# Kernel tuning notes

Measured on AMD Instinct MI355X. Metric: run time of the kernel, lower is better.

## Reference

```python
import jax, jax.numpy as jnp
import numpy as np

EPS = 1e-6
NUM_HEADS = 16


def _layer_norm(x, alpha, beta):
    # Custom LN: unbiased std, divides by (std + eps) -- matches source exactly.
    mean = jnp.mean(x, axis=-1, keepdims=True)
    std = jnp.std(x, axis=-1, keepdims=True, ddof=1)
    return alpha * (x - mean) / (std + EPS) + beta


def _mha(x, wq, bq, wk, bk, wv, bv, wo, bo):
    B, S, D = x.shape
    H = NUM_HEADS
    Dh = D // H
    q = (x @ wq.T + bq).reshape(B, S, H, Dh)
    k = (x @ wk.T + bk).reshape(B, S, H, Dh)
    v = (x @ wv.T + bv).reshape(B, S, H, Dh)
    scores = jnp.einsum('bqhd,bkhd->bhqk', q, k) / jnp.sqrt(jnp.float32(Dh)).astype(x.dtype)
    p = jax.nn.softmax(scores, axis=-1)
    out = jnp.einsum('bhqk,bkhd->bqhd', p, v).reshape(B, S, D)
    return out @ wo.T + bo


def _ffn(x, w1, b1, w2, b2):
    return jax.nn.relu(x @ w1.T + b1) @ w2.T + b2


def setup_inputs() -> dict:
    key = jax.random.key(0)
    ks = jax.random.split(key, 8)
    B, S, D, Hf = 8, 1024, 1024, 4096
    s = lambda d: 1.0 / np.sqrt(d)
    return {
        'x': jax.random.normal(ks[0], (B, S, D), jnp.float32),
        'src_mask': jnp.ones((B, 1, 1, S), jnp.int32),
        'wq': jax.random.normal(ks[1], (D, D), jnp.float32) * s(D),
        'bq': jnp.zeros((D,), jnp.float32),
        'wk': jax.random.normal(ks[2], (D, D), jnp.float32) * s(D),
        'bk': jnp.zeros((D,), jnp.float32),
        'wv': jax.random.normal(ks[3], (D, D), jnp.float32) * s(D),
        'bv': jnp.zeros((D,), jnp.float32),
        'wo': jax.random.normal(ks[4], (D, D), jnp.float32) * s(D),
        'bo': jnp.zeros((D,), jnp.float32),
        'w1': jax.random.normal(ks[5], (Hf, D), jnp.float32) * s(D),
        'b1': jnp.zeros((Hf,), jnp.float32),
        'w2': jax.random.normal(ks[6], (D, Hf), jnp.float32) * s(Hf),
        'b2': jnp.zeros((D,), jnp.float32),
        'alpha': jnp.ones((D,), jnp.float32),
        'beta': jnp.zeros((D,), jnp.float32),
    }


def reference(x, src_mask, wq, bq, wk, bk, wv, bv, wo, bo, w1, b1, w2, b2, alpha, beta):
    # src_mask is unused in the source's attention implementation (faithful).
    # Pre-LN residual block 1: attention (shared LN params alpha/beta).
    x = x + _mha(_layer_norm(x, alpha, beta), wq, bq, wk, bk, wv, bv, wo, bo)
    # Pre-LN residual block 2: feed-forward (same shared LN instance).
    x = x + _ffn(_layer_norm(x, alpha, beta), w1, b1, w2, b2)
    return x
```

## Files before the change

### kernel.cpp

```cpp
#include <hip/hip_runtime.h>
#include <hip/hip_bf16.h>
#include <stdint.h>

typedef __bf16 bf16;
typedef __attribute__((ext_vector_type(8))) __bf16 bf16x8;
typedef __attribute__((ext_vector_type(4))) __bf16 bf16x4;
typedef __attribute__((ext_vector_type(4))) float floatx4;

typedef __attribute__((address_space(3))) uint32_t* lds_u32p;
typedef const __attribute__((address_space(1))) uint32_t* glb_u32p;

__device__ __forceinline__ void gload16(void* lds, const void* g) {
  __builtin_amdgcn_global_load_lds((glb_u32p)(uintptr_t)g,
                                   (lds_u32p)(uintptr_t)lds, 16, 0, 0);
}

__global__ __launch_bounds__(256) void detect_kernel(
    const unsigned short* __restrict__ xr, int* __restrict__ flag) {
  __shared__ int cnt;
  if (threadIdx.x == 0) cnt = 0;
  __syncthreads();
  int c = 0;
  for (int i = threadIdx.x; i < 8192; i += 256) {
    unsigned short e = (xr[i] >> 7) & 0xFF;
    if (e >= 0x90) ++c;
  }
  atomicAdd(&cnt, c);
  __syncthreads();
  if (threadIdx.x == 0) *flag = (cnt > 64) ? 1 : 0;
}

#define NCONV 14
struct ConvArgs {
  const void* src[NCONV];
  bf16* dst[NCONV];
  int nelem[NCONV];
  int bstart[NCONV + 1];
};

__global__ __launch_bounds__(256) void convert_kernel(ConvArgs a, const int* __restrict__ flag) {
  const int isf = *flag;
  const int bx = blockIdx.x;
  int t = 0;
  #pragma unroll
  for (int i = 1; i < NCONV; ++i)
    if (bx >= a.bstart[i]) t = i;
  const int base = (bx - a.bstart[t]) * 2048 + threadIdx.x * 8;
  if (base >= a.nelem[t]) return;
  if (isf) {
    const float* s = (const float*)a.src[t] + base;
    const float4 x0 = *reinterpret_cast<const float4*>(s);
    const float4 x1 = *reinterpret_cast<const float4*>(s + 4);
    bf16x8 o;
    o[0] = (bf16)x0.x; o[1] = (bf16)x0.y; o[2] = (bf16)x0.z; o[3] = (bf16)x0.w;
    o[4] = (bf16)x1.x; o[5] = (bf16)x1.y; o[6] = (bf16)x1.z; o[7] = (bf16)x1.w;
    *reinterpret_cast<bf16x8*>(a.dst[t] + base) = o;
  } else {
    *reinterpret_cast<bf16x8*>(a.dst[t] + base) =
        *reinterpret_cast<const bf16x8*>((const bf16*)a.src[t] + base);
  }
}

__global__ __launch_bounds__(256) void ln_kernel(
    const void* __restrict__ x, const bf16* __restrict__ alpha,
    const bf16* __restrict__ beta, bf16* __restrict__ y,
    const int* __restrict__ flag, int x_ext) {
  const int isf = *flag;
  const int row = blockIdx.x;
  const int tid = threadIdx.x;

  float v0, v1, v2, v3;
  if (x_ext && isf) {
    const float4 xv = *reinterpret_cast<const float4*>(
        (const float*)x + (size_t)row * 1024 + tid * 4);
    v0 = xv.x; v1 = xv.y; v2 = xv.z; v3 = xv.w;
  } else {
    const bf16x4 xv = *reinterpret_cast<const bf16x4*>(
        (const bf16*)x + (size_t)row * 1024 + tid * 4);
    v0 = (float)xv[0]; v1 = (float)xv[1]; v2 = (float)xv[2]; v3 = (float)xv[3];
  }
  float s = v0 + v1 + v2 + v3;
  float ss = v0 * v0 + v1 * v1 + v2 * v2 + v3 * v3;
  #pragma unroll
  for (int off = 32; off > 0; off >>= 1) {
    s += __shfl_down(s, off);
    ss += __shfl_down(ss, off);
  }
  __shared__ float red[8];
  __shared__ float s_mean, s_inv;
  const int w = tid >> 6, lane = tid & 63;
  if (lane == 0) { red[w] = s; red[4 + w] = ss; }
  __syncthreads();
  if (tid == 0) {
    float S = red[0] + red[1] + red[2] + red[3];
    float SS = red[4] + red[5] + red[6] + red[7];
    float mean = S * (1.0f / 1024.0f);
    float var = (SS - 1024.0f * mean * mean) * (1.0f / 1023.0f);
    var = fmaxf(var, 0.0f);
    s_mean = mean;
    s_inv = 1.0f / (sqrtf(var) + 1e-6f);
  }
  __syncthreads();
  const float mean = s_mean, inv = s_inv;
  const bf16x4 av = *reinterpret_cast<const bf16x4*>(alpha + tid * 4);
  const bf16x4 bv = *reinterpret_cast<const bf16x4*>(beta + tid * 4);
  bf16x4 out;
  out[0] = (bf16)((float)av[0] * (v0 - mean) * inv + (float)bv[0]);
  out[1] = (bf16)((float)av[1] * (v1 - mean) * inv + (float)bv[1]);
  out[2] = (bf16)((float)av[2] * (v2 - mean) * inv + (float)bv[2]);
  out[3] = (bf16)((float)av[3] * (v3 - mean) * inv + (float)bv[3]);
  *reinterpret_cast<bf16x4*>(y + (size_t)row * 1024 + tid * 4) = out;
}

template <bool RELU, bool RES>
__global__ __launch_bounds__(256) void gemm_bt(
    const bf16* __restrict__ A, const bf16* __restrict__ W,
    const bf16* __restrict__ bias, const void* __restrict__ res,
    void* __restrict__ C, int M, int N, int K,
    const int* __restrict__ flag, int res_ext, int out_ext, int row0) {
  __shared__ bf16 As[128 * 64];
  __shared__ bf16 Bs[128 * 64];
  const int isf = *flag;
  const int tid = threadIdx.x;
  const int m0 = blockIdx.x * 128, n0 = blockIdx.y * 128;
  const int wave = tid >> 6, lane = tid & 63;
  const int wm = (wave >> 1) * 64, wn = (wave & 1) * 64;
  const int lrow = lane & 15, quad = lane >> 4;

  const int srow = lane >> 3;
  const int gchunk = (lane & 7) ^ srow;
  const bf16* Ab = A + (size_t)m0 * K;
  const bf16* Wb = W + (size_t)n0 * K;

  floatx4 acc[4][4] = {};

  for (int k0 = 0; k0 < K; k0 += 64) {
    __syncthreads();
    #pragma unroll
    for (int t = 0; t < 4; ++t) {
      const int r = t * 32 + wave * 8;
      gload16(&As[r * 64], Ab + (size_t)(r + srow) * K + k0 + gchunk * 8);
      gload16(&Bs[r * 64], Wb + (size_t)(r + srow) * K + k0 + gchunk * 8);
    }
    __syncthreads();

    #pragma unroll
    for (int ks = 0; ks < 2; ++ks) {
      const int cswz = ((ks * 4 + quad) ^ (lrow & 7)) * 8;
      bf16x8 af[4], bw[4];
      #pragma unroll
      for (int i = 0; i < 4; ++i) {
        af[i] = *reinterpret_cast<const bf16x8*>(&As[(wm + i * 16 + lrow) * 64 + cswz]);
        bw[i] = *reinterpret_cast<const bf16x8*>(&Bs[(wn + i * 16 + lrow) * 64 + cswz]);
      }
      #pragma unroll
      for (int i = 0; i < 4; ++i)
        #pragma unroll
        for (int j = 0; j < 4; ++j)
          acc[i][j] = __builtin_amdgcn_mfma_f32_16x16x32_bf16(af[i], bw[j], acc[i][j], 0, 0, 0);
    }
  }

  #pragma unroll
  for (int j = 0; j < 4; ++j) {
    const int col = n0 + wn + j * 16 + lrow;
    const float bv = (float)bias[col];
    #pragma unroll
    for (int i = 0; i < 4; ++i) {
      #pragma unroll
      for (int r = 0; r < 4; ++r) {
        const int row = m0 + wm + i * 16 + quad * 4 + r;
        float v = acc[i][j][r] + bv;
        if (RELU) v = fmaxf(v, 0.0f);
        if (RES) {
          const size_t ridx = (size_t)row * N + col;
          v += (res_ext && isf) ? ((const float*)res)[ridx]
                                : (float)((const bf16*)res)[ridx];
        }
        const size_t oidx = (size_t)(row0 + row) * N + col;
        if (out_ext && isf) ((float*)C)[oidx] = v;
        else ((bf16*)C)[oidx] = (bf16)v;
      }
    }
  }
}

template <bool RELU, bool RES>
__global__ __launch_bounds__(256) void gemm_n64(
    const bf16* __restrict__ A, const bf16* __restrict__ W,
    const bf16* __restrict__ bias, const void* __restrict__ res,
    void* __restrict__ C, int M, int N, int K,
    const int* __restrict__ flag, int res_ext, int out_ext, int row0) {
  __shared__ bf16 As[128 * 64];
  __shared__ bf16 Bs[64 * 64];
  const int isf = *flag;
  const int tid = threadIdx.x;
  const int m0 = blockIdx.x * 128, n0 = blockIdx.y * 64;
  const int wave = tid >> 6, lane = tid & 63;
  const int wm = (wave >> 1) * 64, wn = (wave & 1) * 32;
  const int lrow = lane & 15, quad = lane >> 4;

  const int srow = lane >> 3;
  const int gchunk = (lane & 7) ^ srow;
  const bf16* Ab = A + (size_t)m0 * K;
  const bf16* Wb = W + (size_t)n0 * K;

  floatx4 acc[4][2] = {};

  for (int k0 = 0; k0 < K; k0 += 64) {
    __syncthreads();
    #pragma unroll
    for (int t = 0; t < 4; ++t) {
      const int r = t * 32 + wave * 8;
      gload16(&As[r * 64], Ab + (size_t)(r + srow) * K + k0 + gchunk * 8);
    }
    #pragma unroll
    for (int t = 0; t < 2; ++t) {
      const int r = t * 32 + wave * 8;
      gload16(&Bs[r * 64], Wb + (size_t)(r + srow) * K + k0 + gchunk * 8);
    }
    __syncthreads();

    #pragma unroll
    for (int ks = 0; ks < 2; ++ks) {
      const int cswz = ((ks * 4 + quad) ^ (lrow & 7)) * 8;
      bf16x8 af[4], bw[2];
      #pragma unroll
      for (int i = 0; i < 4; ++i)
        af[i] = *reinterpret_cast<const bf16x8*>(&As[(wm + i * 16 + lrow) * 64 + cswz]);
      #pragma unroll
      for (int j = 0; j < 2; ++j)
        bw[j] = *reinterpret_cast<const bf16x8*>(&Bs[(wn + j * 16 + lrow) * 64 + cswz]);
      #pragma unroll
      for (int i = 0; i < 4; ++i)
        #pragma unroll
        for (int j = 0; j < 2; ++j)
          acc[i][j] = __builtin_amdgcn_mfma_f32_16x16x32_bf16(af[i], bw[j], acc[i][j], 0, 0, 0);
    }
  }

  #pragma unroll
  for (int j = 0; j < 2; ++j) {
    const int col = n0 + wn + j * 16 + lrow;
    const float bv = (float)bias[col];
    #pragma unroll
    for (int i = 0; i < 4; ++i) {
      #pragma unroll
      for (int r = 0; r < 4; ++r) {
        const int row = m0 + wm + i * 16 + quad * 4 + r;
        float v = acc[i][j][r] + bv;
        if (RELU) v = fmaxf(v, 0.0f);
        if (RES) {
          const size_t ridx = (size_t)row * N + col;
          v += (res_ext && isf) ? ((const float*)res)[ridx]
                                : (float)((const bf16*)res)[ridx];
        }
        const size_t oidx = (size_t)(row0 + row) * N + col;
        if (out_ext && isf) ((float*)C)[oidx] = v;
        else ((bf16*)C)[oidx] = (bf16)v;
      }
    }
  }
}

__global__ __launch_bounds__(512, 2) void gemm_ffn1_256(
    const bf16* __restrict__ A, const bf16* __restrict__ W,
    const bf16* __restrict__ bias, bf16* __restrict__ C) {
  constexpr int K = 1024, N = 4096, NK = K / 64;
  __shared__ bf16 As[2][256 * 64];
  __shared__ bf16 Bs[2][256 * 64];
  const int tid = threadIdx.x;
  const int wave = tid >> 6, lane = tid & 63;
  const int m0 = blockIdx.x * 256, n0 = blockIdx.y * 256;
  const int wm = (wave >> 2) * 128;
  const int wn = (wave & 3) * 64;
  const int lrow = lane & 15, quad = lane >> 4;
  const int srow = lane >> 3;
  const int gchunk = (lane & 7) ^ srow;
  const bf16* Ab = A + (size_t)m0 * K;
  const bf16* Wb = W + (size_t)n0 * K;
  const int awr = wave * 32;

  floatx4 acc[8][4] = {};

  auto piece = [&](int kt, int nb, int p) {
    const bf16* G = (p < 2) ? Ab : Wb;
    bf16* L = (p < 2) ? &As[nb][0] : &Bs[nb][0];
    #pragma unroll
    for (int t = (p & 1) * 2; t < (p & 1) * 2 + 2; ++t) {
      const int r = awr + t * 8;
      gload16(L + r * 64, G + (size_t)(r + srow) * K + kt * 64 + gchunk * 8);
    }
  };

  piece(0, 0, 0); piece(0, 0, 1); piece(0, 0, 2); piece(0, 0, 3);

  for (int kt = 0; kt < NK; ++kt) {
    const int cur = kt & 1, nb = cur ^ 1;
    const bool pre = (kt + 1 < NK);

    __builtin_amdgcn_sched_barrier(0);
    __builtin_amdgcn_s_barrier();
    __builtin_amdgcn_sched_barrier(0);
    if (pre) {
      piece(kt + 1, nb, 0);
      asm volatile("s_waitcnt vmcnt(2)" ::: "memory");
    } else {
      asm volatile("s_waitcnt vmcnt(0)" ::: "memory");
    }
    __builtin_amdgcn_sched_barrier(0);
    __builtin_amdgcn_s_barrier();
    __builtin_amdgcn_sched_barrier(0);

    bf16x8 bw[4][2];
    #pragma unroll
    for (int j = 0; j < 4; ++j) {
      const int row = wn + j * 16 + lrow;
      #pragma unroll
      for (int ks = 0; ks < 2; ++ks) {
        const int c = (ks * 4 + quad) ^ (lrow & 7);
        bw[j][ks] = *reinterpret_cast<const bf16x8*>(&Bs[cur][row * 64 + c * 8]);
      }
    }
    #pragma unroll
    for (int p = 0; p < 4; ++p) {
      bf16x8 af[2][2];
      #pragma unroll
      for (int il = 0; il < 2; ++il) {
        const int row = wm + (p * 2 + il) * 16 + lrow;
        #pragma unroll
        for (int ks = 0; ks < 2; ++ks) {
          const int c = (ks * 4 + quad) ^ (lrow & 7);
          af[il][ks] = *reinterpret_cast<const bf16x8*>(&As[cur][row * 64 + c * 8]);
        }
      }
      if (pre && p < 3) piece(kt + 1, nb, p + 1);
      __builtin_amdgcn_s_setprio(1);
      #pragma unroll
      for (int il = 0; il < 2; ++il)
        #pragma unroll
        for (int j = 0; j < 4; ++j)
          #pragma unroll
          for (int ks = 0; ks < 2; ++ks)
            acc[p * 2 + il][j] = __builtin_amdgcn_mfma_f32_16x16x32_bf16(
                af[il][ks], bw[j][ks], acc[p * 2 + il][j], 0, 0, 0);
      __builtin_amdgcn_s_setprio(0);
    }
  }

  #pragma unroll
  for (int j = 0; j < 4; ++j) {
    const int col = n0 + wn + j * 16 + lrow;
    const float bv = (float)bias[col];
    #pragma unroll
    for (int i = 0; i < 8; ++i) {
      #pragma unroll
      for (int r = 0; r < 4; ++r) {
        const int row = m0 + wm + i * 16 + quad * 4 + r;
        C[(size_t)row * N + col] = (bf16)fmaxf(acc[i][j][r] + bv, 0.0f);
      }
    }
  }
}

__global__ __launch_bounds__(512, 2) void gemm_qkv256(
    const bf16* __restrict__ A, const bf16* __restrict__ W,
    const bf16* __restrict__ bias,
    bf16* __restrict__ Oq, bf16* __restrict__ Ok, bf16* __restrict__ Ov) {
  constexpr int K = 1024, NK = K / 64;
  __shared__ bf16 As[2][256 * 64];
  __shared__ bf16 Bs[2][256 * 64];
  const int tid = threadIdx.x;
  const int wave = tid >> 6, lane = tid & 63;
  const int m0 = blockIdx.x * 256, n0 = blockIdx.y * 256;
  const int wm = (wave >> 2) * 128;
  const int wn = (wave & 3) * 64;
  const int lrow = lane & 15, quad = lane >> 4;
  const int srow = lane >> 3;
  const int gchunk = (lane & 7) ^ srow;
  const bf16* Ab = A + (size_t)m0 * K;
  const bf16* Wb = W + (size_t)n0 * K;
  const int awr = wave * 32;

  floatx4 acc[8][4] = {};

  auto piece = [&](int kt, int nb, int p) {
    const bf16* G = (p < 2) ? Ab : Wb;
    bf16* L = (p < 2) ? &As[nb][0] : &Bs[nb][0];
    #pragma unroll
    for (int t = (p & 1) * 2; t < (p & 1) * 2 + 2; ++t) {
      const int r = awr + t * 8;
      gload16(L + r * 64, G + (size_t)(r + srow) * K + kt * 64 + gchunk * 8);
    }
  };

  piece(0, 0, 0); piece(0, 0, 1); piece(0, 0, 2); piece(0, 0, 3);

  for (int kt = 0; kt < NK; ++kt) {
    const int cur = kt & 1, nb = cur ^ 1;
    const bool pre = (kt + 1 < NK);

    __builtin_amdgcn_sched_barrier(0);
    __builtin_amdgcn_s_barrier();
    __builtin_amdgcn_sched_barrier(0);
    if (pre) {
      piece(kt + 1, nb, 0);
      asm volatile("s_waitcnt vmcnt(2)" ::: "memory");
    } else {
      asm volatile("s_waitcnt vmcnt(0)" ::: "memory");
    }
    __builtin_amdgcn_sched_barrier(0);
    __builtin_amdgcn_s_barrier();
    __builtin_amdgcn_sched_barrier(0);

    bf16x8 bw[4][2];
    #pragma unroll
    for (int j = 0; j < 4; ++j) {
      const int row = wn + j * 16 + lrow;
      #pragma unroll
      for (int ks = 0; ks < 2; ++ks) {
        const int c = (ks * 4 + quad) ^ (lrow & 7);
        bw[j][ks] = *reinterpret_cast<const bf16x8*>(&Bs[cur][row * 64 + c * 8]);
      }
    }
    #pragma unroll
    for (int p = 0; p < 4; ++p) {
      bf16x8 af[2][2];
      #pragma unroll
      for (int il = 0; il < 2; ++il) {
        const int row = wm + (p * 2 + il) * 16 + lrow;
        #pragma unroll
        for (int ks = 0; ks < 2; ++ks) {
          const int c = (ks * 4 + quad) ^ (lrow & 7);
          af[il][ks] = *reinterpret_cast<const bf16x8*>(&As[cur][row * 64 + c * 8]);
        }
      }
      if (pre && p < 3) piece(kt + 1, nb, p + 1);
      __builtin_amdgcn_s_setprio(1);
      #pragma unroll
      for (int il = 0; il < 2; ++il)
        #pragma unroll
        for (int j = 0; j < 4; ++j)
          #pragma unroll
          for (int ks = 0; ks < 2; ++ks)
            acc[p * 2 + il][j] = __builtin_amdgcn_mfma_f32_16x16x32_bf16(
                af[il][ks], bw[j][ks], acc[p * 2 + il][j], 0, 0, 0);
      __builtin_amdgcn_s_setprio(0);
    }
  }

  #pragma unroll
  for (int j = 0; j < 4; ++j) {
    const int gcol = n0 + wn + j * 16 + lrow;
    bf16* dst = (gcol < 1024) ? Oq : (gcol < 2048) ? Ok : Ov;
    const int col = gcol & 1023;
    const float bv = (float)bias[gcol];
    #pragma unroll
    for (int i = 0; i < 8; ++i) {
      #pragma unroll
      for (int r = 0; r < 4; ++r) {
        const int row = m0 + wm + i * 16 + quad * 4 + r;
        dst[(size_t)row * 1024 + col] = (bf16)(acc[i][j][r] + bv);
      }
    }
  }
}

template <bool RELU, bool RES>
__global__ __launch_bounds__(512, 2) void gemm_big(
    const bf16* __restrict__ A, const bf16* __restrict__ W,
    const bf16* __restrict__ bias, const void* __restrict__ res,
    void* __restrict__ C, int M, int N, int K,
    const int* __restrict__ flag, int res_ext, int out_ext) {
  __shared__ bf16 As[2][256 * 64];
  __shared__ bf16 Bs[2][128 * 64];
  const int isf = *flag;
  const int tid = threadIdx.x;
  const int wave = tid >> 6, lane = tid & 63;
  const int m0 = blockIdx.x * 256, n0 = blockIdx.y * 128;
  const int wm = (wave & 3) * 64;
  const int wn = (wave >> 2) * 64;
  const int lrow = lane & 15, quad = lane >> 4;
  const int srow = lane >> 3;
  const int gchunk = (lane & 7) ^ srow;
  const bf16* Ab = A + (size_t)m0 * K;
  const bf16* Wb = W + (size_t)n0 * K;
  const int awr = wave * 32;
  const int bwr = wave * 16;

  floatx4 acc[4][4] = {};

  auto piece = [&](int kt, int nb, int p) {
    if (p < 2) {
      const int base = awr + p * 16;
      #pragma unroll
      for (int t = 0; t < 2; ++t) {
        const int r = base + t * 8;
        gload16(&As[nb][r * 64], Ab + (size_t)(r + srow) * K + kt * 64 + gchunk * 8);
      }
    } else {
      #pragma unroll
      for (int t = 0; t < 2; ++t) {
        const int r = bwr + t * 8;
        gload16(&Bs[nb][r * 64], Wb + (size_t)(r + srow) * K + kt * 64 + gchunk * 8);
      }
    }
  };

  const int nk = K >> 6;
  piece(0, 0, 0); piece(0, 0, 1); piece(0, 0, 2);

  for (int kt = 0; kt < nk; ++kt) {
    const int cur = kt & 1, nb = cur ^ 1;
    const bool pre = (kt + 1 < nk);

    __builtin_amdgcn_sched_barrier(0);
    __builtin_amdgcn_s_barrier();
    __builtin_amdgcn_sched_barrier(0);
    if (pre) {
      piece(kt + 1, nb, 0);
      asm volatile("s_waitcnt vmcnt(2)" ::: "memory");
    } else {
      asm volatile("s_waitcnt vmcnt(0)" ::: "memory");
    }
    __builtin_amdgcn_sched_barrier(0);
    __builtin_amdgcn_s_barrier();
    __builtin_amdgcn_sched_barrier(0);

    bf16x8 bw[4][2];
    #pragma unroll
    for (int j = 0; j < 4; ++j) {
      const int row = wn + j * 16 + lrow;
      #pragma unroll
      for (int ks = 0; ks < 2; ++ks) {
        const int c = (ks * 4 + quad) ^ (lrow & 7);
        bw[j][ks] = *reinterpret_cast<const bf16x8*>(&Bs[cur][row * 64 + c * 8]);
      }
    }
    #pragma unroll
    for (int p = 0; p < 4; ++p) {
      bf16x8 af[2];
      {
        const int row = wm + p * 16 + lrow;
        #pragma unroll
        for (int ks = 0; ks < 2; ++ks) {
          const int c = (ks * 4 + quad) ^ (lrow & 7);
          af[ks] = *reinterpret_cast<const bf16x8*>(&As[cur][row * 64 + c * 8]);
        }
      }
      if (pre && p < 2) piece(kt + 1, nb, p + 1);
      __builtin_amdgcn_s_setprio(1);
      #pragma unroll
      for (int j = 0; j < 4; ++j)
        #pragma unroll
        for (int ks = 0; ks < 2; ++ks)
          acc[p][j] = __builtin_amdgcn_mfma_f32_16x16x32_bf16(
              af[ks], bw[j][ks], acc[p][j], 0, 0, 0);
      __builtin_amdgcn_s_setprio(0);
    }
  }

  #pragma unroll
  for (int j = 0; j < 4; ++j) {
    const int col = n0 + wn + j * 16 + lrow;
    const float bv = (float)bias[col];
    #pragma unroll
    for (int i = 0; i < 4; ++i) {
      #pragma unroll
      for (int r = 0; r < 4; ++r) {
        const int row = m0 + wm + i * 16 + quad * 4 + r;
        float v = acc[i][j][r] + bv;
        if (RELU) v = fmaxf(v, 0.0f);
        if (RES) {
          const size_t ridx = (size_t)row * N + col;
          v += (res_ext && isf) ? ((const float*)res)[ridx]
                                : (float)((const bf16*)res)[ridx];
        }
        const size_t oidx = (size_t)row * N + col;
        if (out_ext && isf) ((float*)C)[oidx] = v;
        else ((bf16*)C)[oidx] = (bf16)v;
      }
    }
  }
}

__global__ __launch_bounds__(256) void attn_kernel(
    const bf16* __restrict__ Qg, const bf16* __restrict__ Kg,
    const bf16* __restrict__ Vg, bf16* __restrict__ Og) {
  __shared__ bf16 Ks[64][72];
  __shared__ bf16 Vts[64][72];
  __shared__ bf16 Ps[4][32][72];

  const int tid = threadIdx.x, wave = tid >> 6, lane = tid & 63;
  const int lrow = lane & 15, quad = lane >> 4;
  const int bq = blockIdx.x, h = blockIdx.y, b = blockIdx.z;
  const int q0 = bq * 128 + wave * 32;

  bf16x8 qa[2][2];
  #pragma unroll
  for (int t = 0; t < 2; ++t) {
    const bf16* qbase = Qg + (size_t)(b * 1024 + q0 + t * 16 + lrow) * 1024 + h * 64;
    qa[t][0] = *reinterpret_cast<const bf16x8*>(qbase + quad * 8);
    qa[t][1] = *reinterpret_cast<const bf16x8*>(qbase + 32 + quad * 8);
  }

  const int skp = tid >> 2, sdd = (tid & 3) * 16;
  const int vkp = tid & 63, vdg = wave * 16;

  floatx4 o[2][4] = {};
  float lsum[2][4] = {};

  for (int kc = 0; kc < 1024; kc += 64) {
    __syncthreads();
    {
      const bf16* ksrc = Kg + (size_t)(b * 1024 + kc + skp) * 1024 + h * 64 + sdd;
      *reinterpret_cast<bf16x8*>(&Ks[skp][sdd]) = *reinterpret_cast<const bf16x8*>(ksrc);
      *reinterpret_cast<bf16x8*>(&Ks[skp][sdd + 8]) = *reinterpret_cast<const bf16x8*>(ksrc + 8);

      const bf16* vsrc = Vg + (size_t)(b * 1024 + kc + vkp) * 1024 + h * 64 + vdg;
      bf16x8 v0 = *reinterpret_cast<const bf16x8*>(vsrc);
      bf16x8 v1 = *reinterpret_cast<const bf16x8*>(vsrc + 8);
      #pragma unroll
      for (int j = 0; j < 8; ++j) {
        Vts[vdg + j][vkp] = v0[j];
        Vts[vdg + 8 + j][vkp] = v1[j];
      }
    }
    __syncthreads();

    #pragma unroll
    for (int t = 0; t < 2; ++t) {
      floatx4 s[4] = {};
      #pragma unroll
      for (int kt = 0; kt < 4; ++kt) {
        bf16x8 kb0 = *reinterpret_cast<const bf16x8*>(&Ks[kt * 16 + lrow][quad * 8]);
        bf16x8 kb1 = *reinterpret_cast<const bf16x8*>(&Ks[kt * 16 + lrow][32 + quad * 8]);
        s[kt] = __builtin_amdgcn_mfma_f32_16x16x32_bf16(qa[t][0], kb0, s[kt], 0, 0, 0);
        s[kt] = __builtin_amdgcn_mfma_f32_16x16x32_bf16(qa[t][1], kb1, s[kt], 0, 0, 0);
      }
      #pragma unroll
      for (int r = 0; r < 4; ++r) {
        const float p0 = __expf(s[0][r] * 0.125f);
        const float p1 = __expf(s[1][r] * 0.125f);
        const float p2 = __expf(s[2][r] * 0.125f);
        const float p3 = __expf(s[3][r] * 0.125f);
        lsum[t][r] += (p0 + p1) + (p2 + p3);
        const int qr = t * 16 + quad * 4 + r;
        Ps[wave][qr][lrow] = (bf16)p0;
        Ps[wave][qr][16 + lrow] = (bf16)p1;
        Ps[wave][qr][32 + lrow] = (bf16)p2;
        Ps[wave][qr][48 + lrow] = (bf16)p3;
      }
    }

    __builtin_amdgcn_wave_barrier();

    #pragma unroll
    for (int t = 0; t < 2; ++t) {
      const bf16x8 pf0 = *reinterpret_cast<const bf16x8*>(&Ps[wave][t * 16 + lrow][quad * 8]);
      const bf16x8 pf1 = *reinterpret_cast<const bf16x8*>(&Ps[wave][t * 16 + lrow][32 + quad * 8]);
      #pragma unroll
      for (int j = 0; j < 4; ++j) {
        bf16x8 vb0 = *reinterpret_cast<const bf16x8*>(&Vts[j * 16 + lrow][quad * 8]);
        bf16x8 vb1 = *reinterpret_cast<const bf16x8*>(&Vts[j * 16 + lrow][32 + quad * 8]);
        o[t][j] = __builtin_amdgcn_mfma_f32_16x16x32_bf16(pf0, vb0, o[t][j], 0, 0, 0);
        o[t][j] = __builtin_amdgcn_mfma_f32_16x16x32_bf16(pf1, vb1, o[t][j], 0, 0, 0);
      }
    }
  }

  #pragma unroll
  for (int t = 0; t < 2; ++t) {
    #pragma unroll
    for (int r = 0; r < 4; ++r) {
      float l = lsum[t][r];
      #pragma unroll
      for (int off = 1; off < 16; off <<= 1) l += __shfl_xor(l, off);
      const float inv = 1.0f / l;
      const size_t qrow = (size_t)(b * 1024 + q0 + t * 16 + quad * 4 + r);
      #pragma unroll
      for (int j = 0; j < 4; ++j)
        Og[qrow * 1024 + h * 64 + j * 16 + lrow] = (bf16)(o[t][j][r] * inv);
    }
  }
}

extern "C" void kernel_launch(void* const* d_in, const int* in_sizes, int n_in,
                              void* d_out, int out_size, void* d_ws, size_t ws_size,
                              hipStream_t stream) {
  const void* p[16];
  {
    int j = 0;
    for (int i = 0; i < 16; ++i) {
      if (i == 1) {
        if (j < n_in && in_sizes[j] == 8192) p[i] = d_in[j++];
        else p[i] = nullptr;
        continue;
      }
      p[i] = (j < n_in) ? d_in[j++] : nullptr;
    }
  }
  const void* x = p[0];

  char* ws = (char*)d_ws;
  int* flag = (int*)ws;
  char* wsc = ws + 256;

  const int wsz[NCONV] = {1048576, 1048576, 1048576, 1048576, 4194304, 4194304,
                          1024, 1024, 1024, 1024, 4096, 1024, 1024, 1024};
  const int wsrc[NCONV] = {2, 4, 6, 8, 10, 12, 3, 5, 7, 9, 11, 13, 14, 15};
  ConvArgs ca;
  bf16* cptr[NCONV];
  size_t off = 0;
  int bacc = 0;
  for (int i = 0; i < NCONV; ++i) {
    cptr[i] = (bf16*)(wsc + off);
    off += (size_t)wsz[i] * sizeof(bf16);
    ca.src[i] = p[wsrc[i]];
    ca.dst[i] = cptr[i];
    ca.nelem[i] = wsz[i];
    ca.bstart[i] = bacc;
    bacc += (wsz[i] + 2047) / 2048;
  }
  ca.bstart[NCONV] = bacc;
  const bf16 *wq_c = cptr[0], *wo_c = cptr[3];
  const bf16 *w1_c = cptr[4], *w2_c = cptr[5];
  const bf16 *bq_c = cptr[6], *bo_c = cptr[9];
  const bf16 *b1_c = cptr[10], *b2_c = cptr[11], *al_c = cptr[12], *be_c = cptr[13];

  char* base = wsc + ((off + 255) & ~(size_t)255);
  const size_t SZ = (size_t)8192 * 1024 * sizeof(bf16);
  bf16* s1 = (bf16*)(base);
  bf16* s0 = (bf16*)(base + SZ);
  bf16* s2 = (bf16*)(base + 2 * SZ);
  bf16* s3 = (bf16*)(base + 3 * SZ);
  bf16* Kb = (bf16*)d_out;

  const int M = 8192, D = 1024, HF = 4096;

  detect_kernel<<<1, 256, 0, stream>>>((const unsigned short*)x, flag);
  convert_kernel<<<bacc, 256, 0, stream>>>(ca, flag);
  ln_kernel<<<8192, 256, 0, stream>>>(x, al_c, be_c, s0, flag, 1);
  gemm_qkv256<<<dim3(M / 256, 3072 / 256), 512, 0, stream>>>(
      s0, wq_c, bq_c, s1, Kb, s2);
  attn_kernel<<<dim3(8, 16, 8), 256, 0, stream>>>(s1, Kb, s2, s3);
  gemm_big<false, true><<<dim3(M / 256, D / 128), 512, 0, stream>>>(
      s3, wo_c, bo_c, x, s1, M, D, D, flag, 1, 0);
  ln_kernel<<<8192, 256, 0, stream>>>(s1, al_c, be_c, s0, flag, 0);

  const size_t used = (size_t)(base - ws) + 4 * SZ;
  if (ws_size >= used + (size_t)M * HF * sizeof(bf16)) {
    bf16* Hf = (bf16*)(base + 4 * SZ);
    gemm_ffn1_256<<<dim3(M / 256, HF / 256), 512, 0, stream>>>(s0, w1_c, b1_c, Hf);
    gemm_big<false, true><<<dim3(M / 256, D / 128), 512, 0, stream>>>(
        Hf, w2_c, b2_c, s1, d_out, M, D, HF, flag, 0, 1);
  } else {
    bf16* H = s2;
    for (int hh = 0; hh < 2; ++hh) {
      const size_t ro = (size_t)hh * 4096 * 1024;
      gemm_bt<true, false><<<dim3(32, 32), 256, 0, stream>>>(
          s0 + ro, w1_c, b1_c, nullptr, H, 4096, HF, D, flag, 0, 0, 0);
      gemm_n64<false, true><<<dim3(32, D / 64), 256, 0, stream>>>(
          H, w2_c, b2_c, s1 + ro, d_out, 4096, D, HF, flag, 0, 1, hh * 4096);
    }
  }
}
```

Measured before the change: 499.2 us.

## Restructure GEMM inner loop into k-slice phases with barrier-synchronized MFMA clusters

```diff
diff --git a/kernel.cpp b/kernel.cpp
--- a/kernel.cpp
+++ b/kernel.cpp
@@ -527,36 +527,39 @@
     __builtin_amdgcn_s_barrier();
     __builtin_amdgcn_sched_barrier(0);
 
-    bf16x8 bw[4][2];
-    #pragma unroll
-    for (int j = 0; j < 4; ++j) {
-      const int row = wn + j * 16 + lrow;
-      #pragma unroll
-      for (int ks = 0; ks < 2; ++ks) {
-        const int c = (ks * 4 + quad) ^ (lrow & 7);
-        bw[j][ks] = *reinterpret_cast<const bf16x8*>(&Bs[cur][row * 64 + c * 8]);
-      }
-    }
-    #pragma unroll
-    for (int p = 0; p < 4; ++p) {
-      bf16x8 af[2];
-      {
-        const int row = wm + p * 16 + lrow;
+    bf16x8 bw[4], af[2];
+    #pragma unroll
+    for (int ks = 0; ks < 2; ++ks) {
+      const int c = ((ks * 4 + quad) ^ (lrow & 7)) * 8;
+      #pragma unroll
+      for (int mh = 0; mh < 2; ++mh) {
+        if (mh == 0) {
+          #pragma unroll
+          for (int j = 0; j < 4; ++j)
+            bw[j] = *reinterpret_cast<const bf16x8*>(
+                &Bs[cur][(wn + j * 16 + lrow) * 64 + c]);
+        }
         #pragma unroll
-        for (int ks = 0; ks < 2; ++ks) {
-          const int c = (ks * 4 + quad) ^ (lrow & 7);
-          af[ks] = *reinterpret_cast<const bf16x8*>(&As[cur][row * 64 + c * 8]);
-        }
-      }
-      if (pre && p < 2) piece(kt + 1, nb, p + 1);
-      __builtin_amdgcn_s_setprio(1);
-      #pragma unroll
-      for (int j = 0; j < 4; ++j)
+        for (int il = 0; il < 2; ++il)
+          af[il] = *reinterpret_cast<const bf16x8*>(
+              &As[cur][(wm + (mh * 2 + il) * 16 + lrow) * 64 + c]);
+        if (pre && ks == 0) piece(kt + 1, nb, mh + 1);
+        __builtin_amdgcn_sched_barrier(0);
+        __builtin_amdgcn_s_barrier();
+        asm volatile("s_waitcnt lgkmcnt(0)" ::: "memory");
+        __builtin_amdgcn_sched_barrier(0);
+        __builtin_amdgcn_s_setprio(1);
         #pragma unroll
-        for (int ks = 0; ks < 2; ++ks)
-          acc[p][j] = __builtin_amdgcn_mfma_f32_16x16x32_bf16(
-              af[ks], bw[j][ks], acc[p][j], 0, 0, 0);
-      __builtin_amdgcn_s_setprio(0);
+        for (int il = 0; il < 2; ++il)
+          #pragma unroll
+          for (int j = 0; j < 4; ++j)
+            acc[mh * 2 + il][j] = __builtin_amdgcn_mfma_f32_16x16x32_bf16(
+                af[il], bw[j], acc[mh * 2 + il][j], 0, 0, 0);
+        __builtin_amdgcn_s_setprio(0);
+        __builtin_amdgcn_sched_barrier(0);
+        __builtin_amdgcn_s_barrier();
+        __builtin_amdgcn_sched_barrier(0);
+      }
     }
   }
 
```

After: 523.1 us. +4.8%, slower.
